# Kernel tuning notes

Hardware: AMD Instinct MI355X
Metric: run time of the kernel (lower is better)

The kernel has to match this reference:

```python
import jax, jax.numpy as jnp
import numpy as np

WIN = 7
K1, K2 = 0.01, 0.03
IN_CHAN = 8
NP_WIN = WIN * WIN
COV_NORM = NP_WIN / (NP_WIN - 1)


def _box_filter(x, w, groups):
    return jax.lax.conv_general_dilated(
        x, w, window_strides=(1, 1), padding='VALID',
        feature_group_count=groups,
        dimension_numbers=('NCHW', 'OIHW', 'NCHW'))


def setup_inputs() -> dict:
    key = jax.random.key(0)
    kx, ky = jax.random.split(key)
    X = jax.random.uniform(kx, (32, IN_CHAN, 320, 320), dtype=jnp.float32)
    Y = jax.random.uniform(ky, (32, IN_CHAN, 320, 320), dtype=jnp.float32)
    data_range = jnp.ones((1,), dtype=jnp.float32)
    w = jnp.ones((IN_CHAN, 1, WIN, WIN), dtype=jnp.float32) / NP_WIN
    return {"X": X, "Y": Y, "data_range": data_range, "w": w}


def reference(X, Y, data_range, w):
    C1 = (K1 * data_range) ** 2
    C2 = (K2 * data_range) ** 2
    ux = _box_filter(X, w, IN_CHAN)
    uy = _box_filter(Y, w, IN_CHAN)
    uxx = _box_filter(X * X, w, IN_CHAN)
    uyy = _box_filter(Y * Y, w, IN_CHAN)
    uxy = _box_filter(X * Y, w, IN_CHAN)
    vx = COV_NORM * (uxx - ux * ux)
    vy = COV_NORM * (uyy - uy * uy)
    vxy = COV_NORM * (uxy - ux * uy)
    A1 = 2 * ux * uy + C1
    A2 = 2 * vxy + C2
    B1 = ux ** 2 + uy ** 2 + C1
    B2 = vx + vy + C2
    S = A1 * A2 / (B1 * B2 + 1e-8)
    return 1 - S.mean()
```

## Files before the change

kernel.cpp:

```cpp
#include <hip/hip_runtime.h>

#define H 320
#define W 320
#define OH 314
#define OW 314
#define NIMG 256
#define STRIP_OUT 42
#define NSTRIP 8
#define NGRP 3
#define GRPW 122

__device__ __forceinline__ float ssim_val(float sxs, float sys, float sxxs,
                                          float syys, float sxys,
                                          float w0, float C1, float C2) {
    const float COV = 49.0f / 48.0f;
    float ux  = sxs  * w0, uy  = sys  * w0;
    float uxx = sxxs * w0, uyy = syys * w0, uxy = sxys * w0;
    float vx  = COV * (uxx - ux * ux);
    float vy  = COV * (uyy - uy * uy);
    float vxy = COV * (uxy - ux * uy);
    float A1 = 2.f * ux * uy + C1;
    float A2 = 2.f * vxy + C2;
    float B1 = ux * ux + uy * uy + C1;
    float B2 = vx + vy + C2;
    float den = B1 * B2 + 1e-8f;
    float inv = __builtin_amdgcn_rcpf(den);
    inv = inv * (2.f - den * inv);
    return (A1 * A2) * inv;
}

#define HSUM(v2, e, o)                                   \
{                                                        \
    float p  = v2.x + v2.y;                              \
    float p1 = __shfl_down(p, 1);                        \
    float p2 = __shfl_down(p, 2);                        \
    float p3 = __shfl_down(p, 3);                        \
    float q  = __shfl_down(v2.x, 3);                     \
    e = p + p1 + p2 + q;                                 \
    o = v2.y + p1 + p2 + p3;                             \
}

#define ROW_BODY(P, I, DOEMIT)                                             \
{                                                                          \
    const int rr   = min(r0 + (I), H - 1);                                 \
    const int rofs = rr * W + cl;                                          \
    const float2 xn = *(const float2*)(Xb + rofs);                         \
    const float2 yn = *(const float2*)(Yb + rofs);                         \
    const float2 xo = rx[P];                                               \
    const float2 yo = ry[P];                                               \
    sx.x  += xn.x - xo.x;            sx.y  += xn.y - xo.y;                 \
    sy.x  += yn.x - yo.x;            sy.y  += yn.y - yo.y;                 \
    sxx.x += xn.x*xn.x - xo.x*xo.x;  sxx.y += xn.y*xn.y - xo.y*xo.y;       \
    syy.x += yn.x*yn.x - yo.x*yo.x;  syy.y += yn.y*yn.y - yo.y*yo.y;       \
    sxy.x += xn.x*yn.x - xo.x*yo.x;  sxy.y += xn.y*yn.y - xo.y*yo.y;       \
    rx[P] = xn; ry[P] = yn;                                                \
    if (DOEMIT) {                                                          \
        const int orow = r0 + (I) - 6;                                     \
        if (orow < OH) {                                                   \
            float ex, oxv, ey, oyv, exx, oxx, eyy, oyy, exy, oxy;          \
            HSUM(sx,  ex,  oxv)                                            \
            HSUM(sy,  ey,  oyv)                                            \
            HSUM(sxx, exx, oxx)                                            \
            HSUM(syy, eyy, oyy)                                            \
            HSUM(sxy, exy, oxy)                                            \
            float S0 = ssim_val(ex,  ey,  exx, eyy, exy, w0, C1, C2);      \
            float S1 = ssim_val(oxv, oyv, oxx, oyy, oxy, w0, C1, C2);      \
            acc += (v0ok ? S0 : 0.f) + (v1ok ? S1 : 0.f);                  \
        }                                                                  \
    }                                                                      \
}

__global__ __launch_bounds__(256) void ssim_slide_kernel(
    const float* __restrict__ X, const float* __restrict__ Y,
    const float* __restrict__ dr_p, const float* __restrict__ w_p,
    double* __restrict__ accum)
{
    const int t    = threadIdx.x;
    const int lane = t & 63;
    const int wave = t >> 6;

    const int bid  = blockIdx.x;
    const int img  = bid / (NGRP * 2);
    const int rem  = bid - img * (NGRP * 2);
    const int grp  = rem >> 1;
    const int half = rem & 1;
    const int strip = half * 4 + wave;
    const int r0    = strip * STRIP_OUT;

    const int cbase = grp * GRPW;
    const int c0 = cbase + 2 * lane;
    const int cl = min(c0, W - 2);

    const float* __restrict__ Xb = X + (size_t)img * (H * W);
    const float* __restrict__ Yb = Y + (size_t)img * (H * W);

    const float dr = dr_p[0];
    const float w0 = w_p[0];
    const float C1 = (0.01f * dr) * (0.01f * dr);
    const float C2 = (0.03f * dr) * (0.03f * dr);

    const bool v0ok = (lane <= 60) && (c0     < OW);
    const bool v1ok = (lane <= 60) && (c0 + 1 < OW);

    float2 rx[7], ry[7];
#pragma unroll
    for (int i = 0; i < 7; ++i) { rx[i] = make_float2(0.f, 0.f); ry[i] = make_float2(0.f, 0.f); }
    float2 sx  = make_float2(0.f, 0.f), sy  = make_float2(0.f, 0.f);
    float2 sxx = make_float2(0.f, 0.f), syy = make_float2(0.f, 0.f);
    float2 sxy = make_float2(0.f, 0.f);
    float acc = 0.f;

    ROW_BODY(0, 0, false)
    ROW_BODY(1, 1, false)
    ROW_BODY(2, 2, false)
    ROW_BODY(3, 3, false)
    ROW_BODY(4, 4, false)
    ROW_BODY(5, 5, false)
    ROW_BODY(6, 6, true)

    for (int j = 1; j < 6; ++j) {
        const int base = j * 7;
        ROW_BODY(0, base + 0, true)
        ROW_BODY(1, base + 1, true)
        ROW_BODY(2, base + 2, true)
        ROW_BODY(3, base + 3, true)
        ROW_BODY(4, base + 4, true)
        ROW_BODY(5, base + 5, true)
        ROW_BODY(6, base + 6, true)
    }

    ROW_BODY(0, 42, true)
    ROW_BODY(1, 43, true)
    ROW_BODY(2, 44, true)
    ROW_BODY(3, 45, true)
    ROW_BODY(4, 46, true)
    ROW_BODY(5, 47, true)

#pragma unroll
    for (int off = 32; off > 0; off >>= 1)
        acc += __shfl_down(acc, off);

    __shared__ float wsum[4];
    if (lane == 0) wsum[wave] = acc;
    __syncthreads();
    if (t == 0) {
        float s = wsum[0] + wsum[1] + wsum[2] + wsum[3];
        atomicAdd(accum, (double)s);
    }
}

__global__ void ssim_finalize_kernel(const double* __restrict__ accum,
                                     float* __restrict__ out)
{
    const double cnt = (double)NIMG * (double)(OH * OW);
    out[0] = 1.0f - (float)(accum[0] / cnt);
}

extern "C" void kernel_launch(void* const* d_in, const int* in_sizes, int n_in,
                              void* d_out, int out_size, void* d_ws, size_t ws_size,
                              hipStream_t stream) {
    const float* X  = (const float*)d_in[0];
    const float* Y  = (const float*)d_in[1];
    const float* dr = (const float*)d_in[2];
    const float* w  = (const float*)d_in[3];
    double* accum   = (double*)d_ws;
    float* out      = (float*)d_out;

    hipMemsetAsync(accum, 0, sizeof(double), stream);

    const int nblocks = NIMG * NGRP * 2;
    ssim_slide_kernel<<<nblocks, 256, 0, stream>>>(X, Y, dr, w, accum);
    ssim_finalize_kernel<<<1, 1, 0, stream>>>(accum, out);
}
```

Before: 268.4 us.

## Shorten row strips for more blocks, cheaper horizontal sums, fuse finalize via ticket

Reduces each wave's strip from 42 to 16 output rows and grows the grid to five row-blocks per column group, aiming for more parallel waves and better latency hiding. The horizontal 7-tap sum is rewritten as an 8-wide shuffle sum minus an edge element, cutting shuffles. The separate finalize kernel is removed; the last block, found via an atomic ticket, writes the result. The trade-off is more halo rows reloaded per output row.

New measurement: 406.3 us. +51.4%, slower.

```diff
diff --git a/kernel.cpp b/kernel.cpp
--- a/kernel.cpp
+++ b/kernel.cpp
@@ -5,10 +5,12 @@
 #define OH 314
 #define OW 314
 #define NIMG 256
-#define STRIP_OUT 42
-#define NSTRIP 8
+#define SOUT 16
+#define NSTRIP 20
 #define NGRP 3
 #define GRPW 122
+#define NBLK 5
+#define NBLOCKS (NIMG * NGRP * NBLK)
 
 __device__ __forceinline__ float ssim_val(float sxs, float sys, float sxxs,
                                           float syys, float sxys,
@@ -29,15 +31,14 @@
     return (A1 * A2) * inv;
 }
 
-#define HSUM(v2, e, o)                                   \
+#define HSUM3(v2, e, o)                                  \
 {                                                        \
-    float p  = v2.x + v2.y;                              \
-    float p1 = __shfl_down(p, 1);                        \
-    float p2 = __shfl_down(p, 2);                        \
-    float p3 = __shfl_down(p, 3);                        \
-    float q  = __shfl_down(v2.x, 3);                     \
-    e = p + p1 + p2 + q;                                 \
-    o = v2.y + p1 + p2 + p3;                             \
+    float P_ = v2.x + v2.y;                              \
+    float t_ = P_ + __shfl_down(P_, 1);                  \
+    float S8 = t_ + __shfl_down(t_, 2);                  \
+    float o3 = __shfl_down(v2.y, 3);                     \
+    e = S8 - o3;                                         \
+    o = S8 - v2.x;                                       \
 }
 
 #define ROW_BODY(P, I, DOEMIT)                                             \
@@ -58,11 +59,11 @@
         const int orow = r0 + (I) - 6;                                     \
         if (orow < OH) {                                                   \
             float ex, oxv, ey, oyv, exx, oxx, eyy, oyy, exy, oxy;          \
-            HSUM(sx,  ex,  oxv)                                            \
-            HSUM(sy,  ey,  oyv)                                            \
-            HSUM(sxx, exx, oxx)                                            \
-            HSUM(syy, eyy, oyy)                                            \
-            HSUM(sxy, exy, oxy)                                            \
+            HSUM3(sx,  ex,  oxv)                                           \
+            HSUM3(sy,  ey,  oyv)                                           \
+            HSUM3(sxx, exx, oxx)                                           \
+            HSUM3(syy, eyy, oyy)                                           \
+            HSUM3(sxy, exy, oxy)                                           \
             float S0 = ssim_val(ex,  ey,  exx, eyy, exy, w0, C1, C2);      \
             float S1 = ssim_val(oxv, oyv, oxx, oyy, oxy, w0, C1, C2);      \
             acc += (v0ok ? S0 : 0.f) + (v1ok ? S1 : 0.f);                  \
@@ -73,19 +74,20 @@
 __global__ __launch_bounds__(256) void ssim_slide_kernel(
     const float* __restrict__ X, const float* __restrict__ Y,
     const float* __restrict__ dr_p, const float* __restrict__ w_p,
-    double* __restrict__ accum)
+    double* __restrict__ accum, unsigned int* __restrict__ ticket,
+    float* __restrict__ out)
 {
     const int t    = threadIdx.x;
     const int lane = t & 63;
     const int wave = t >> 6;
 
-    const int bid  = blockIdx.x;
-    const int img  = bid / (NGRP * 2);
-    const int rem  = bid - img * (NGRP * 2);
-    const int grp  = rem >> 1;
-    const int half = rem & 1;
-    const int strip = half * 4 + wave;
-    const int r0    = strip * STRIP_OUT;
+    const int bid = blockIdx.x;
+    const int img = bid / (NGRP * NBLK);
+    const int rem = bid - img * (NGRP * NBLK);
+    const int grp = rem / NBLK;
+    const int blk = rem - grp * NBLK;
+    const int strip = blk * 4 + wave;
+    const int r0    = strip * SOUT;
 
     const int cbase = grp * GRPW;
     const int c0 = cbase + 2 * lane;
@@ -110,31 +112,28 @@
     float2 sxy = make_float2(0.f, 0.f);
     float acc = 0.f;
 
-    ROW_BODY(0, 0, false)
-    ROW_BODY(1, 1, false)
-    ROW_BODY(2, 2, false)
-    ROW_BODY(3, 3, false)
-    ROW_BODY(4, 4, false)
-    ROW_BODY(5, 5, false)
-    ROW_BODY(6, 6, true)
-
-    for (int j = 1; j < 6; ++j) {
-        const int base = j * 7;
-        ROW_BODY(0, base + 0, true)
-        ROW_BODY(1, base + 1, true)
-        ROW_BODY(2, base + 2, true)
-        ROW_BODY(3, base + 3, true)
-        ROW_BODY(4, base + 4, true)
-        ROW_BODY(5, base + 5, true)
-        ROW_BODY(6, base + 6, true)
-    }
-
-    ROW_BODY(0, 42, true)
-    ROW_BODY(1, 43, true)
-    ROW_BODY(2, 44, true)
-    ROW_BODY(3, 45, true)
-    ROW_BODY(4, 46, true)
-    ROW_BODY(5, 47, true)
+    ROW_BODY(0, 0,  false)
+    ROW_BODY(1, 1,  false)
+    ROW_BODY(2, 2,  false)
+    ROW_BODY(3, 3,  false)
+    ROW_BODY(4, 4,  false)
+    ROW_BODY(5, 5,  false)
+    ROW_BODY(6, 6,  true)
+    ROW_BODY(0, 7,  true)
+    ROW_BODY(1, 8,  true)
+    ROW_BODY(2, 9,  true)
+    ROW_BODY(3, 10, true)
+    ROW_BODY(4, 11, true)
+    ROW_BODY(5, 12, true)
+    ROW_BODY(6, 13, true)
+    ROW_BODY(0, 14, true)
+    ROW_BODY(1, 15, true)
+    ROW_BODY(2, 16, true)
+    ROW_BODY(3, 17, true)
+    ROW_BODY(4, 18, true)
+    ROW_BODY(5, 19, true)
+    ROW_BODY(6, 20, true)
+    ROW_BODY(0, 21, true)
 
 #pragma unroll
     for (int off = 32; off > 0; off >>= 1)
@@ -146,14 +145,14 @@
     if (t == 0) {
         float s = wsum[0] + wsum[1] + wsum[2] + wsum[3];
         atomicAdd(accum, (double)s);
+        __threadfence();
+        unsigned int prev = atomicAdd(ticket, 1u);
+        if (prev == (unsigned int)(NBLOCKS - 1)) {
+            double tot = atomicAdd(accum, 0.0);
+            const double cnt = (double)NIMG * (double)(OH * OW);
+            out[0] = 1.0f - (float)(tot / cnt);
+        }
     }
-}
-
-__global__ void ssim_finalize_kernel(const double* __restrict__ accum,
-                                     float* __restrict__ out)
-{
-    const double cnt = (double)NIMG * (double)(OH * OW);
-    out[0] = 1.0f - (float)(accum[0] / cnt);
 }
 
 extern "C" void kernel_launch(void* const* d_in, const int* in_sizes, int n_in,
@@ -163,12 +162,11 @@
     const float* Y  = (const float*)d_in[1];
     const float* dr = (const float*)d_in[2];
     const float* w  = (const float*)d_in[3];
-    double* accum   = (double*)d_ws;
-    float* out      = (float*)d_out;
+    double* accum        = (double*)d_ws;
+    unsigned int* ticket = (unsigned int*)((char*)d_ws + 8);
+    float* out           = (float*)d_out;
 
-    hipMemsetAsync(accum, 0, sizeof(double), stream);
+    hipMemsetAsync(d_ws, 0, 16, stream);
 
-    const int nblocks = NIMG * NGRP * 2;
-    ssim_slide_kernel<<<nblocks, 256, 0, stream>>>(X, Y, dr, w, accum);
-    ssim_finalize_kernel<<<1, 1, 0, stream>>>(accum, out);
+    ssim_slide_kernel<<<NBLOCKS, 256, 0, stream>>>(X, Y, dr, w, accum, ticket, out);
 }
```
